# Kernel tuning notes

Measured on AMD Instinct MI355X. Metric: run time of the kernel, lower is better.

## Reference

```python
import jax, jax.numpy as jnp
import numpy as np
from jax import lax

N, HW = 64, 240
C0, C1, C2, C3 = 3, 32, 64, 128
HEAD = 1280


def _conv(x, w, stride, pad):
    return lax.conv_general_dilated(
        x, w, (stride, stride), [(pad, pad), (pad, pad)],
        dimension_numbers=("NCHW", "OIHW", "NCHW"))


def _cbr(x, w, alpha, beta, stride, pad, do_relu=True):
    # conv2d with pre-folded BN: y = conv(x,w)*alpha + beta, then ReLU
    y = _conv(x, w, stride, pad)
    y = y * alpha[None, :, None, None] + beta[None, :, None, None]
    return jnp.maximum(y, 0.0) if do_relu else y


def setup_inputs() -> dict:
    key = jax.random.key(0)
    ks = jax.random.split(key, 13)
    f32 = jnp.float32
    inp = {
        "x": jax.random.normal(ks[0], (N, C0, HW, HW), dtype=f32),
        # stem 3x3 s2: 3 -> 32
        "w_stem": jax.random.normal(ks[1], (C1, C0, 3, 3), dtype=f32) * 0.1,
        "a_stem": jax.random.uniform(ks[2], (C1,), dtype=f32, minval=0.5, maxval=1.5),
        "b_stem": jax.random.normal(ks[3], (C1,), dtype=f32) * 0.1,
        # mid 3x3 s2: 32 -> 64
        "w1": jax.random.normal(ks[4], (C2, C1, 3, 3), dtype=f32) * 0.05,
        "a1": jax.random.uniform(ks[5], (C2,), dtype=f32, minval=0.5, maxval=1.5),
        "b1": jax.random.normal(ks[6], (C2,), dtype=f32) * 0.1,
        # pointwise 1x1 s1: 64 -> 128
        "w2": jax.random.normal(ks[7], (C3, C2, 1, 1), dtype=f32) * 0.05,
        "a2": jax.random.uniform(ks[8], (C3,), dtype=f32, minval=0.5, maxval=1.5),
        "b2": jax.random.normal(ks[9], (C3,), dtype=f32) * 0.1,
        # head: GAP + GEMV (w2d [Cout, Cin]) + BN-fold + ReLU
        "w_head": jax.random.normal(ks[10], (HEAD, C3), dtype=f32) * 0.05,
        "a_head": jax.random.uniform(ks[11], (HEAD,), dtype=f32, minval=0.5, maxval=1.5),
        "b_head": jax.random.normal(ks[12], (HEAD,), dtype=f32) * 0.1,
    }
    return inp


def reference(x, w_stem, a_stem, b_stem, w1, a1, b1, w2, a2, b2,
              w_head, a_head, b_head):
    h = _cbr(x, w_stem, a_stem, b_stem, stride=2, pad=1)   # [N,32,120,120]
    h = _cbr(h, w1, a1, b1, stride=2, pad=1)               # [N,64,60,60]
    h = _cbr(h, w2, a2, b2, stride=1, pad=0)               # [N,128,60,60]
    # head: global average pool + GEMV + folded-BN affine + ReLU
    gap = h.mean(axis=(2, 3))                              # [N,128]
    out = jnp.einsum("nc,oc->no", gap, w_head)             # [N,1280]
    out = out * a_head[None, :] + b_head[None, :]
    return jnp.maximum(out, 0.0)
```

## Files before the change

### kernel.cpp

```cpp
#include <hip/hip_runtime.h>

#define N_    64
#define HW_   240
#define H1_   120
#define H2_   60
#define C0_   3
#define C1_   32
#define C2_   64
#define C3_   128
#define HEAD_ 1280

typedef unsigned short US;
typedef short bf16x8 __attribute__((ext_vector_type(8)));
typedef float f32x16 __attribute__((ext_vector_type(16)));

__device__ __forceinline__ US f2bf(float f) {
  union { float f; unsigned u; } v; v.f = f;
  unsigned r = v.u + 0x7FFF + ((v.u >> 16) & 1);
  return (US)(r >> 16);
}

#define H1Q_ROW 3968
#define H1Q_PL  1984

#define ZCHN   368
#define ZTOT   (64 * ZCHN * 4)
__global__ __launch_bounds__(256) void k0_prep(
    const float* __restrict__ w1, const float* __restrict__ w2,
    const float* __restrict__ w0,
    US* __restrict__ h1q, US* __restrict__ wt1, US* __restrict__ wt2,
    US* __restrict__ wt0, float* __restrict__ gap) {
  int gid = blockIdx.x * 256 + threadIdx.x;
  if (gid < ZTOT) {
    int c = gid >> 2, q = gid & 3;
    int n = c / ZCHN, cc = c % ZCHN;
    long off; int y;
    if (cc < 124)      { y = 0;   off = (long)cc * 32; }
    else if (cc < 248) { y = 121; off = (long)(cc - 124) * 32; }
    else               { y = cc - 247; off = H1Q_PL; }
    uint4 z; z.x = z.y = z.z = z.w = 0u;
    *(uint4*)(h1q + ((long)(n * 122 + y)) * H1Q_ROW + off + q * 8) = z;
  } else if (gid < ZTOT + 18432) {
    int e = gid - ZTOT;
    int oc = e / 288, ic = (e / 9) % 32, ky = (e / 3) % 3, kx = e % 3;
    wt1[((ky * 3 + kx) * 64 + oc) * 32 + ic] = f2bf(w1[e]);
  } else if (gid < ZTOT + 18432 + 8192) {
    int e = gid - (ZTOT + 18432);
    wt2[e] = f2bf(w2[e]);
  } else if (gid < ZTOT + 18432 + 8192 + 1024) {
    int e = gid - (ZTOT + 18432 + 8192);
    int oc = e >> 5, k = e & 31;
    wt0[e] = (k < 27) ? f2bf(w0[oc * 27 + k]) : (US)0;
  } else if (gid < ZTOT + 18432 + 8192 + 1024 + 8192) {
    gap[gid - (ZTOT + 18432 + 8192 + 1024)] = 0.f;
  }
}

#define XSW 244
__global__ __launch_bounds__(256) void k1_mfma(
    const float* __restrict__ x, const US* __restrict__ wt0,
    const float* __restrict__ alpha, const float* __restrict__ beta,
    US* __restrict__ h1q) {
  __shared__ float xs[3 * 3 * XSW];
  __shared__ US ot[128 * 32];
  int y = blockIdx.x, n = blockIdx.y;
  int iy0 = 2 * y - 1;
  const float* xn = x + (long)n * C0_ * HW_ * HW_;
  for (int e = threadIdx.x; e < 3 * 3 * XSW; e += 256) {
    int w244 = e % XSW, rc = e / XSW;
    int ic = rc / 3, r = rc % 3;
    int iy = iy0 + r, ix = w244 - 1;
    float v = 0.f;
    if (iy >= 0 && ix >= 0 && ix < HW_)
      v = xn[(long)ic * HW_ * HW_ + iy * HW_ + ix];
    xs[e] = v;
  }
  __syncthreads();

  int t = threadIdx.x, wv = t >> 6, l = t & 63;
  int lane31 = l & 31, half = l >> 5;
  int ox = wv * 32 + lane31;
  int oxc = ox < H1_ ? ox : (H1_ - 1);

  float fa[16];
#pragma unroll
  for (int m = 0; m < 2; m++)
#pragma unroll
    for (int j = 0; j < 8; j++) {
      int k = m * 16 + half * 8 + j;
      float v = 0.f;
      if (k < 27) {
        int ic = k / 9, rem = k - ic * 9;
        int ky = rem / 3, kx = rem - ky * 3;
        v = xs[(ic * 3 + ky) * XSW + 2 * oxc + kx];
      }
      fa[m * 8 + j] = v;
    }
  bf16x8 a0, a1;
#pragma unroll
  for (int j = 0; j < 8; j++) {
    a0[j] = (short)f2bf(fa[j]);
    a1[j] = (short)f2bf(fa[8 + j]);
  }
  const US* wb = wt0 + lane31 * 32 + half * 8;
  bf16x8 b0 = *(const bf16x8*)(wb);
  bf16x8 b1 = *(const bf16x8*)(wb + 16);

  f32x16 acc;
#pragma unroll
  for (int i = 0; i < 16; i++) acc[i] = 0.f;
  acc = __builtin_amdgcn_mfma_f32_32x32x16_bf16(a0, b0, acc, 0, 0, 0);
  acc = __builtin_amdgcn_mfma_f32_32x32x16_bf16(a1, b1, acc, 0, 0, 0);

  int oc = lane31;
  float al = alpha[oc], be = beta[oc];
#pragma unroll
  for (int r = 0; r < 16; r++) {
    int row = (r & 3) + 8 * (r >> 2) + 4 * half;
    float v = fmaxf(fmaf(acc[r], al, be), 0.f);
    ot[(wv * 32 + row) * 32 + oc] = f2bf(v);
  }
  __syncthreads();

  long rowb = ((long)(n * 122 + y + 1)) * H1Q_ROW;
  for (int u = t; u < 480; u += 256) {
    int px = u >> 2, q = u & 3;
    int pl = px & 1;
    int m = (px + 1) >> 1;
    long addr = rowb + (pl ? H1Q_PL : 0) + (long)m * 32 + q * 8;
    *(uint4*)(h1q + addr) = *(const uint4*)(ot + px * 32 + q * 8);
  }
}

#define TS 72
__global__ __launch_bounds__(256) void k2_fused(
    const US* __restrict__ h1q, const US* __restrict__ wt1,
    const US* __restrict__ wt2,
    const float* __restrict__ a1, const float* __restrict__ b1,
    const float* __restrict__ a2, const float* __restrict__ b2,
    float* __restrict__ gap) {
  __shared__ US tile[128 * TS];
  int n = blockIdx.y, tileb = blockIdx.x;
  int t = threadIdx.x, w = t >> 6, l = t & 63;
  int wm = w & 1, wn = w >> 1;
  int lane31 = l & 31, half = l >> 5;
  int oc = wn * 32 + lane31;

  int pxb0 = tileb * 128 + wm * 64;
  int pxb1 = pxb0 + 32;
  int p0 = pxb0 + lane31; int pc0 = p0 < 3600 ? p0 : 3599;
  int p1 = pxb1 + lane31; int pc1 = p1 < 3600 ? p1 : 3599;
  int y0 = pc0 / 60, xx0 = pc0 % 60;
  int y1 = pc1 / 60, xx1 = pc1 % 60;

  f32x16 accA, accB;
#pragma unroll
  for (int i = 0; i < 16; i++) { accA[i] = 0.f; accB[i] = 0.f; }

#pragma unroll
  for (int ky = 0; ky < 3; ky++) {
    const US* c0a1 = h1q + ((long)(n * 122 + 2 * y0 + ky)) * H1Q_ROW
                         + (long)xx0 * 32 + half * 8;
    const US* c1a1 = h1q + ((long)(n * 122 + 2 * y1 + ky)) * H1Q_ROW
                         + (long)xx1 * 32 + half * 8;
    const US* wk = wt1 + (ky * 3) * (64 * 32) + oc * 32 + half * 8;
#pragma unroll
    for (int kx = 0; kx < 3; kx++) {
      long aoff = (kx == 1) ? 0 : (kx == 0 ? H1Q_PL : (H1Q_PL + 32));
      const US* bp = wk + kx * (64 * 32);
#pragma unroll
      for (int c = 0; c < 2; c++) {
        bf16x8 bv  = *(const bf16x8*)(bp + c * 16);
        bf16x8 av0 = *(const bf16x8*)(c0a1 + aoff + c * 16);
        bf16x8 av1 = *(const bf16x8*)(c1a1 + aoff + c * 16);
        accA = __builtin_amdgcn_mfma_f32_32x32x16_bf16(av0, bv, accA, 0, 0, 0);
        accB = __builtin_amdgcn_mfma_f32_32x32x16_bf16(av1, bv, accB, 0, 0, 0);
      }
    }
  }
  {
    float al = a1[oc], be = b1[oc];
#pragma unroll
    for (int r = 0; r < 16; r++) {
      int row = (r & 3) + 8 * (r >> 2) + 4 * half;
      float vA = fmaxf(fmaf(accA[r], al, be), 0.f);
      float vB = fmaxf(fmaf(accB[r], al, be), 0.f);
      tile[(wm * 64 + row) * TS + oc] = f2bf(vA);
      tile[(wm * 64 + 32 + row) * TS + oc] = f2bf(vB);
    }
  }
  __syncthreads();

  int base_px = tileb * 128 + w * 32;
  const US* abase2 = tile + (w * 32 + lane31) * TS + half * 8;
  bf16x8 af[4];
#pragma unroll
  for (int c = 0; c < 4; c++) af[c] = *(const bf16x8*)(abase2 + c * 16);

#pragma unroll
  for (int nt = 0; nt < 4; nt++) {
    int oc2 = nt * 32 + lane31;
    const US* bb = wt2 + oc2 * 64 + half * 8;
    f32x16 acc2;
#pragma unroll
    for (int i = 0; i < 16; i++) acc2[i] = 0.f;
#pragma unroll
    for (int c = 0; c < 4; c++) {
      bf16x8 bv = *(const bf16x8*)(bb + c * 16);
      acc2 = __builtin_amdgcn_mfma_f32_32x32x16_bf16(af[c], bv, acc2, 0, 0, 0);
    }
    float al2 = a2[oc2], be2 = b2[oc2];
    float s = 0.f;
    if (base_px + 31 < 3600) {
#pragma unroll
      for (int r = 0; r < 16; r++) s += fmaxf(fmaf(acc2[r], al2, be2), 0.f);
    } else {
#pragma unroll
      for (int r = 0; r < 16; r++) {
        int row = (r & 3) + 8 * (r >> 2) + 4 * half;
        if (base_px + row < 3600) s += fmaxf(fmaf(acc2[r], al2, be2), 0.f);
      }
    }
    s += __shfl_xor(s, 32);
    if (half == 0) atomicAdd(gap + n * C3_ + oc2, s);
  }
}

__global__ __launch_bounds__(256) void k4_head(
    const float* __restrict__ gap, const float* __restrict__ wh,
    const float* __restrict__ alpha, const float* __restrict__ beta,
    float* __restrict__ out) {
  __shared__ float g[C3_];
  int n = blockIdx.y;
  int o = blockIdx.x * 256 + threadIdx.x;
  if (threadIdx.x < C3_)
    g[threadIdx.x] = gap[n * C3_ + threadIdx.x] * (1.f / 3600.f);
  __syncthreads();
  const float* wr = wh + (long)o * C3_;
  float acc = 0.f;
#pragma unroll 8
  for (int c = 0; c < C3_; c += 4) {
    float4 wv = *(const float4*)(wr + c);
    acc = fmaf(wv.x, g[c],     acc);
    acc = fmaf(wv.y, g[c + 1], acc);
    acc = fmaf(wv.z, g[c + 2], acc);
    acc = fmaf(wv.w, g[c + 3], acc);
  }
  out[n * HEAD_ + o] = fmaxf(fmaf(acc, alpha[o], beta[o]), 0.f);
}

extern "C" void kernel_launch(void* const* d_in, const int* in_sizes, int n_in,
                              void* d_out, int out_size, void* d_ws,
                              size_t ws_size, hipStream_t stream) {
  const float* x      = (const float*)d_in[0];
  const float* w_stem = (const float*)d_in[1];
  const float* a_stem = (const float*)d_in[2];
  const float* b_stem = (const float*)d_in[3];
  const float* w1     = (const float*)d_in[4];
  const float* a1     = (const float*)d_in[5];
  const float* b1     = (const float*)d_in[6];
  const float* w2     = (const float*)d_in[7];
  const float* a2     = (const float*)d_in[8];
  const float* b2     = (const float*)d_in[9];
  const float* wh     = (const float*)d_in[10];
  const float* ah     = (const float*)d_in[11];
  const float* bh     = (const float*)d_in[12];
  float* out = (float*)d_out;

  US* h1q = (US*)d_ws;
  US* wt1 = h1q + (size_t)N_ * 122 * H1Q_ROW;
  US* wt2 = wt1 + 9 * 64 * 32;
  US* wt0 = wt2 + C3_ * C2_;
  float* gap = (float*)(wt0 + 1024);

  {
    int total = ZTOT + 18432 + 8192 + 1024 + 8192;
    k0_prep<<<(total + 255) / 256, 256, 0, stream>>>(w1, w2, w_stem, h1q,
                                                     wt1, wt2, wt0, gap);
  }
  {
    dim3 grid(H1_, N_);
    k1_mfma<<<grid, 256, 0, stream>>>(x, wt0, a_stem, b_stem, h1q);
  }
  {
    dim3 grid(29, N_);
    k2_fused<<<grid, 256, 0, stream>>>(h1q, wt1, wt2, a1, b1, a2, b2, gap);
  }
  {
    dim3 grid(HEAD_ / 256, N_);
    k4_head<<<grid, 256, 0, stream>>>(gap, wh, ah, bh, out);
  }
}
```

Baseline: 183.0 us.

## Enlarge per-block work in stem and fused conv kernels with more MFMA tiles per wave

The stem kernel now handles 4 output rows per block (one per wave), each wave doing 4 column tiles. It loads a 9-row input strip shared across those rows and writes outputs straight to global memory instead of staging them through shared memory. The fused conv kernel doubles its pixel tile to 256, so each wave keeps 4 accumulators that reuse each loaded weight vector. The pointwise stage reuses its B fragments across two pixel sub-tiles. This cuts block count and launch overhead and improves weight reuse, at the cost of more registers, lower occupancy, and scattered 2-byte global stores in the stem.

```diff
diff --git a/kernel.cpp b/kernel.cpp
--- a/kernel.cpp
+++ b/kernel.cpp
@@ -61,15 +61,14 @@
     const float* __restrict__ x, const US* __restrict__ wt0,
     const float* __restrict__ alpha, const float* __restrict__ beta,
     US* __restrict__ h1q) {
-  __shared__ float xs[3 * 3 * XSW];
-  __shared__ US ot[128 * 32];
-  int y = blockIdx.x, n = blockIdx.y;
-  int iy0 = 2 * y - 1;
+  __shared__ float xs[3 * 9 * XSW];
+  int bx = blockIdx.x, n = blockIdx.y;
+  int iy0 = 8 * bx - 1;
   const float* xn = x + (long)n * C0_ * HW_ * HW_;
-  for (int e = threadIdx.x; e < 3 * 3 * XSW; e += 256) {
-    int w244 = e % XSW, rc = e / XSW;
-    int ic = rc / 3, r = rc % 3;
-    int iy = iy0 + r, ix = w244 - 1;
+  for (int e = threadIdx.x; e < 3 * 9 * XSW; e += 256) {
+    int col = e % XSW, seg = e / XSW;
+    int ic = seg / 9, rr = seg % 9;
+    int iy = iy0 + rr, ix = col - 1;
     float v = 0.f;
     if (iy >= 0 && ix >= 0 && ix < HW_)
       v = xn[(long)ic * HW_ * HW_ + iy * HW_ + ix];
@@ -79,56 +78,64 @@
 
   int t = threadIdx.x, wv = t >> 6, l = t & 63;
   int lane31 = l & 31, half = l >> 5;
-  int ox = wv * 32 + lane31;
-  int oxc = ox < H1_ ? ox : (H1_ - 1);
-
-  float fa[16];
-#pragma unroll
-  for (int m = 0; m < 2; m++)
-#pragma unroll
-    for (int j = 0; j < 8; j++) {
-      int k = m * 16 + half * 8 + j;
-      float v = 0.f;
-      if (k < 27) {
-        int ic = k / 9, rem = k - ic * 9;
-        int ky = rem / 3, kx = rem - ky * 3;
-        v = xs[(ic * 3 + ky) * XSW + 2 * oxc + kx];
-      }
-      fa[m * 8 + j] = v;
-    }
-  bf16x8 a0, a1;
-#pragma unroll
-  for (int j = 0; j < 8; j++) {
-    a0[j] = (short)f2bf(fa[j]);
-    a1[j] = (short)f2bf(fa[8 + j]);
-  }
+  int y = bx * 4 + wv;
+  int oc = lane31;
+
   const US* wb = wt0 + lane31 * 32 + half * 8;
   bf16x8 b0 = *(const bf16x8*)(wb);
   bf16x8 b1 = *(const bf16x8*)(wb + 16);
 
-  f32x16 acc;
-#pragma unroll
-  for (int i = 0; i < 16; i++) acc[i] = 0.f;
-  acc = __builtin_amdgcn_mfma_f32_32x32x16_bf16(a0, b0, acc, 0, 0, 0);
-  acc = __builtin_amdgcn_mfma_f32_32x32x16_bf16(a1, b1, acc, 0, 0, 0);
-
-  int oc = lane31;
+  int joff[16]; bool jok[16];
+#pragma unroll
+  for (int m = 0; m < 2; m++)
+#pragma unroll
+    for (int j = 0; j < 8; j++) {
+      int k = m * 16 + half * 8 + j;
+      bool ok = k < 27;
+      int ic = ok ? k / 9 : 0;
+      int rem = k - ic * 9;
+      int ky = rem / 3, kx = rem - ky * 3;
+      joff[m * 8 + j] = (ic * 9 + 2 * wv + ky) * XSW + kx;
+      jok[m * 8 + j] = ok;
+    }
+
   float al = alpha[oc], be = beta[oc];
-#pragma unroll
-  for (int r = 0; r < 16; r++) {
-    int row = (r & 3) + 8 * (r >> 2) + 4 * half;
-    float v = fmaxf(fmaf(acc[r], al, be), 0.f);
-    ot[(wv * 32 + row) * 32 + oc] = f2bf(v);
-  }
-  __syncthreads();
-
   long rowb = ((long)(n * 122 + y + 1)) * H1Q_ROW;
-  for (int u = t; u < 480; u += 256) {
-    int px = u >> 2, q = u & 3;
-    int pl = px & 1;
-    int m = (px + 1) >> 1;
-    long addr = rowb + (pl ? H1Q_PL : 0) + (long)m * 32 + q * 8;
-    *(uint4*)(h1q + addr) = *(const uint4*)(ot + px * 32 + q * 8);
+
+  f32x16 acc[4];
+  bf16x8 a0[4], a1[4];
+#pragma unroll
+  for (int c = 0; c < 4; c++) {
+    int ox = c * 32 + lane31;
+    int oxc = ox < H1_ ? ox : (H1_ - 1);
+    int base = 2 * oxc;
+#pragma unroll
+    for (int j = 0; j < 8; j++) {
+      a0[c][j] = (short)(jok[j]     ? f2bf(xs[joff[j] + base])     : 0);
+      a1[c][j] = (short)(jok[8 + j] ? f2bf(xs[joff[8 + j] + base]) : 0);
+    }
+#pragma unroll
+    for (int i = 0; i < 16; i++) acc[c][i] = 0.f;
+  }
+#pragma unroll
+  for (int c = 0; c < 4; c++)
+    acc[c] = __builtin_amdgcn_mfma_f32_32x32x16_bf16(a0[c], b0, acc[c], 0, 0, 0);
+#pragma unroll
+  for (int c = 0; c < 4; c++)
+    acc[c] = __builtin_amdgcn_mfma_f32_32x32x16_bf16(a1[c], b1, acc[c], 0, 0, 0);
+
+#pragma unroll
+  for (int c = 0; c < 4; c++) {
+#pragma unroll
+    for (int r = 0; r < 16; r++) {
+      int row = (r & 3) + 8 * (r >> 2) + 4 * half;
+      int px = c * 32 + row;
+      if (px < H1_) {
+        float v = fmaxf(fmaf(acc[c][r], al, be), 0.f);
+        long addr = rowb + ((px & 1) ? H1Q_PL : 0) + (long)((px + 1) >> 1) * 32 + oc;
+        h1q[addr] = f2bf(v);
+      }
+    }
   }
 }
 
@@ -139,86 +146,99 @@
     const float* __restrict__ a1, const float* __restrict__ b1,
     const float* __restrict__ a2, const float* __restrict__ b2,
     float* __restrict__ gap) {
-  __shared__ US tile[128 * TS];
+  __shared__ US tile[256 * TS];
   int n = blockIdx.y, tileb = blockIdx.x;
   int t = threadIdx.x, w = t >> 6, l = t & 63;
   int wm = w & 1, wn = w >> 1;
   int lane31 = l & 31, half = l >> 5;
   int oc = wn * 32 + lane31;
 
-  int pxb0 = tileb * 128 + wm * 64;
-  int pxb1 = pxb0 + 32;
-  int p0 = pxb0 + lane31; int pc0 = p0 < 3600 ? p0 : 3599;
-  int p1 = pxb1 + lane31; int pc1 = p1 < 3600 ? p1 : 3599;
-  int y0 = pc0 / 60, xx0 = pc0 % 60;
-  int y1 = pc1 / 60, xx1 = pc1 % 60;
-
-  f32x16 accA, accB;
-#pragma unroll
-  for (int i = 0; i < 16; i++) { accA[i] = 0.f; accB[i] = 0.f; }
+  int yy[4], xx[4];
+#pragma unroll
+  for (int c = 0; c < 4; c++) {
+    int p = tileb * 256 + wm * 128 + c * 32 + lane31;
+    int pc = p < 3600 ? p : 3599;
+    yy[c] = pc / 60; xx[c] = pc % 60;
+  }
+
+  f32x16 acc[4];
+#pragma unroll
+  for (int c = 0; c < 4; c++)
+#pragma unroll
+    for (int i = 0; i < 16; i++) acc[c][i] = 0.f;
 
 #pragma unroll
   for (int ky = 0; ky < 3; ky++) {
-    const US* c0a1 = h1q + ((long)(n * 122 + 2 * y0 + ky)) * H1Q_ROW
-                         + (long)xx0 * 32 + half * 8;
-    const US* c1a1 = h1q + ((long)(n * 122 + 2 * y1 + ky)) * H1Q_ROW
-                         + (long)xx1 * 32 + half * 8;
+    const US* ab[4];
+#pragma unroll
+    for (int c = 0; c < 4; c++)
+      ab[c] = h1q + ((long)(n * 122 + 2 * yy[c] + ky)) * H1Q_ROW
+                  + (long)xx[c] * 32 + half * 8;
     const US* wk = wt1 + (ky * 3) * (64 * 32) + oc * 32 + half * 8;
 #pragma unroll
     for (int kx = 0; kx < 3; kx++) {
       long aoff = (kx == 1) ? 0 : (kx == 0 ? H1Q_PL : (H1Q_PL + 32));
       const US* bp = wk + kx * (64 * 32);
 #pragma unroll
-      for (int c = 0; c < 2; c++) {
-        bf16x8 bv  = *(const bf16x8*)(bp + c * 16);
-        bf16x8 av0 = *(const bf16x8*)(c0a1 + aoff + c * 16);
-        bf16x8 av1 = *(const bf16x8*)(c1a1 + aoff + c * 16);
-        accA = __builtin_amdgcn_mfma_f32_32x32x16_bf16(av0, bv, accA, 0, 0, 0);
-        accB = __builtin_amdgcn_mfma_f32_32x32x16_bf16(av1, bv, accB, 0, 0, 0);
+      for (int cc = 0; cc < 2; cc++) {
+        bf16x8 bv = *(const bf16x8*)(bp + cc * 16);
+#pragma unroll
+        for (int c = 0; c < 4; c++) {
+          bf16x8 av = *(const bf16x8*)(ab[c] + aoff + cc * 16);
+          acc[c] = __builtin_amdgcn_mfma_f32_32x32x16_bf16(av, bv, acc[c], 0, 0, 0);
+        }
       }
     }
   }
   {
     float al = a1[oc], be = b1[oc];
 #pragma unroll
-    for (int r = 0; r < 16; r++) {
-      int row = (r & 3) + 8 * (r >> 2) + 4 * half;
-      float vA = fmaxf(fmaf(accA[r], al, be), 0.f);
-      float vB = fmaxf(fmaf(accB[r], al, be), 0.f);
-      tile[(wm * 64 + row) * TS + oc] = f2bf(vA);
-      tile[(wm * 64 + 32 + row) * TS + oc] = f2bf(vB);
-    }
+    for (int c = 0; c < 4; c++)
+#pragma unroll
+      for (int r = 0; r < 16; r++) {
+        int row = (r & 3) + 8 * (r >> 2) + 4 * half;
+        float v = fmaxf(fmaf(acc[c][r], al, be), 0.f);
+        tile[(wm * 128 + c * 32 + row) * TS + oc] = f2bf(v);
+      }
   }
   __syncthreads();
 
-  int base_px = tileb * 128 + w * 32;
-  const US* abase2 = tile + (w * 32 + lane31) * TS + half * 8;
-  bf16x8 af[4];
-#pragma unroll
-  for (int c = 0; c < 4; c++) af[c] = *(const bf16x8*)(abase2 + c * 16);
+  int base_px = tileb * 256 + w * 64;
+  bf16x8 af[2][4];
+#pragma unroll
+  for (int s = 0; s < 2; s++) {
+    const US* ap = tile + (w * 64 + s * 32 + lane31) * TS + half * 8;
+#pragma unroll
+    for (int c = 0; c < 4; c++) af[s][c] = *(const bf16x8*)(ap + c * 16);
+  }
 
 #pragma unroll
   for (int nt = 0; nt < 4; nt++) {
     int oc2 = nt * 32 + lane31;
     const US* bb = wt2 + oc2 * 64 + half * 8;
-    f32x16 acc2;
-#pragma unroll
-    for (int i = 0; i < 16; i++) acc2[i] = 0.f;
-#pragma unroll
-    for (int c = 0; c < 4; c++) {
-      bf16x8 bv = *(const bf16x8*)(bb + c * 16);
-      acc2 = __builtin_amdgcn_mfma_f32_32x32x16_bf16(af[c], bv, acc2, 0, 0, 0);
-    }
+    bf16x8 bv[4];
+#pragma unroll
+    for (int c = 0; c < 4; c++) bv[c] = *(const bf16x8*)(bb + c * 16);
     float al2 = a2[oc2], be2 = b2[oc2];
     float s = 0.f;
-    if (base_px + 31 < 3600) {
-#pragma unroll
-      for (int r = 0; r < 16; r++) s += fmaxf(fmaf(acc2[r], al2, be2), 0.f);
-    } else {
-#pragma unroll
-      for (int r = 0; r < 16; r++) {
-        int row = (r & 3) + 8 * (r >> 2) + 4 * half;
-        if (base_px + row < 3600) s += fmaxf(fmaf(acc2[r], al2, be2), 0.f);
+#pragma unroll
+    for (int st = 0; st < 2; st++) {
+      f32x16 acc2;
+#pragma unroll
+      for (int i = 0; i < 16; i++) acc2[i] = 0.f;
+#pragma unroll
+      for (int c = 0; c < 4; c++)
+        acc2 = __builtin_amdgcn_mfma_f32_32x32x16_bf16(af[st][c], bv[c], acc2, 0, 0, 0);
+      int pxb = base_px + st * 32;
+      if (pxb + 31 < 3600) {
+#pragma unroll
+        for (int r = 0; r < 16; r++) s += fmaxf(fmaf(acc2[r], al2, be2), 0.f);
+      } else {
+#pragma unroll
+        for (int r = 0; r < 16; r++) {
+          int row = (r & 3) + 8 * (r >> 2) + 4 * half;
+          if (pxb + row < 3600) s += fmaxf(fmaf(acc2[r], al2, be2), 0.f);
+        }
       }
     }
     s += __shfl_xor(s, 32);
@@ -279,11 +299,11 @@
                                                      wt1, wt2, wt0, gap);
   }
   {
-    dim3 grid(H1_, N_);
+    dim3 grid(30, N_);
     k1_mfma<<<grid, 256, 0, stream>>>(x, wt0, a_stem, b_stem, h1q);
   }
   {
-    dim3 grid(29, N_);
+    dim3 grid(15, N_);
     k2_fused<<<grid, 256, 0, stream>>>(h1q, wt1, wt2, a1, b1, a2, b2, gap);
   }
   {
```

New measurement: 199.4 us. 1.09x slower.
